# Performance work log

Hardware: AMD Instinct MI355X
Metric: run time of the kernel (lower is better)

The kernel has to match this reference:

```python
import math
import jax, jax.numpy as jnp
import numpy as np

BATCH, SEQ, D_MODEL, NUM_HEADS = 4, 2048, 1024, 16
D_K = D_MODEL // NUM_HEADS


def setup_inputs() -> dict:
    key = jax.random.key(0)
    ks = jax.random.split(key, 11)
    s = 0.02
    inp = {
        'encodings_q': jax.random.normal(ks[0], (BATCH, SEQ, D_MODEL), jnp.float32),
        'encodings_k': jax.random.normal(ks[1], (BATCH, SEQ, D_MODEL), jnp.float32),
        'encodings_v': jax.random.normal(ks[2], (BATCH, SEQ, D_MODEL), jnp.float32),
        # causal mask: True = masked out (matches masked_fill semantics)
        'mask': jnp.broadcast_to(jnp.triu(jnp.ones((SEQ, SEQ), bool), k=1),
                                 (BATCH, SEQ, SEQ)),
        'Wq': jax.random.normal(ks[3], (D_MODEL, D_MODEL), jnp.float32) * s,
        'bq': jnp.zeros((D_MODEL,), jnp.float32),
        'Wk': jax.random.normal(ks[4], (D_MODEL, D_MODEL), jnp.float32) * s,
        'bk': jnp.zeros((D_MODEL,), jnp.float32),
        'Wv': jax.random.normal(ks[5], (D_MODEL, D_MODEL), jnp.float32) * s,
        'bv': jnp.zeros((D_MODEL,), jnp.float32),
        'Wo': jax.random.normal(ks[6], (D_MODEL, D_MODEL), jnp.float32) * s,
        'bo': jnp.zeros((D_MODEL,), jnp.float32),
    }
    return inp


def reference(encodings_q, encodings_k, encodings_v, mask,
              Wq, bq, Wk, bk, Wv, bv, Wo, bo):
    B, S, D = encodings_q.shape
    H, Dk = NUM_HEADS, D_K
    # projections (nn.Linear: x @ W.T + b), split heads -> (B, H, S, Dk)
    q = (encodings_q @ Wq.T + bq).reshape(B, S, H, Dk).transpose(0, 2, 1, 3)
    k = (encodings_k @ Wk.T + bk).reshape(B, S, H, Dk).transpose(0, 2, 1, 3)
    v = (encodings_v @ Wv.T + bv).reshape(B, S, H, Dk).transpose(0, 2, 1, 3)
    scores = jnp.einsum('bhqd,bhkd->bhqk', q, k) / math.sqrt(Dk)
    # mask dim == 3 -> unsqueeze head dim; masked_fill(mask, -1e9)
    scores = jnp.where(mask[:, None, :, :], jnp.float32(-1e9), scores)
    weights = jax.nn.softmax(scores, axis=-1)
    attn = jnp.einsum('bhqk,bhkd->bhqd', weights, v)
    attn = attn.transpose(0, 2, 1, 3).reshape(B, S, D)
    return attn @ Wo.T + bo
```

## Files before the change

### kernel.cpp

```cpp
#include <hip/hip_runtime.h>
#include <hip/hip_bf16.h>
#include <cstdint>

typedef __bf16 bf16;
typedef bf16  bf16x4 __attribute__((ext_vector_type(4)));
typedef bf16  bf16x8 __attribute__((ext_vector_type(8)));
typedef float f32x4  __attribute__((ext_vector_type(4)));

#define MFMA16(a, b, c) __builtin_amdgcn_mfma_f32_16x16x32_bf16((a), (b), (c), 0, 0, 0)

constexpr int BATCH = 4;
constexpr int SEQ   = 2048;
constexpr int DM    = 1024;
constexpr int NH    = 16;
constexpr int DK    = 64;

__device__ __forceinline__ void gld_lds16(const void* g, void* l) {
    __builtin_amdgcn_global_load_lds(
        (const __attribute__((address_space(1))) unsigned int*)(uintptr_t)g,
        (__attribute__((address_space(3))) unsigned int*)(uintptr_t)l,
        16, 0, 0);
}

__device__ __forceinline__ bf16x8 cvt8(const float* __restrict__ p) {
    f32x4 a = *(const f32x4*)p;
    f32x4 b = *(const f32x4*)(p + 4);
    bf16x8 r;
    r[0] = (bf16)a[0]; r[1] = (bf16)a[1]; r[2] = (bf16)a[2]; r[3] = (bf16)a[3];
    r[4] = (bf16)b[0]; r[5] = (bf16)b[1]; r[6] = (bf16)b[2]; r[7] = (bf16)b[3];
    return r;
}

__global__ __launch_bounds__(256)
void cvt_all(const float* __restrict__ xq, const float* __restrict__ xk,
             const float* __restrict__ xv,
             const float* __restrict__ wq, const float* __restrict__ wk,
             const float* __restrict__ wv, const float* __restrict__ wo,
             bf16* __restrict__ X3, bf16* __restrict__ WB)
{
    const int bid = blockIdx.x;
    const float* s;
    bf16* d;
    int local;
    if (bid < 12288) {
        const int which = bid >> 12;
        local = bid & 4095;
        s = (which == 0) ? xq : (which == 1) ? xk : xv;
        d = X3 + (size_t)which * ((size_t)BATCH * SEQ * DM);
    } else {
        const int b2 = bid - 12288;
        const int which = b2 >> 9;
        local = b2 & 511;
        s = (which == 0) ? wq : (which == 1) ? wk : (which == 2) ? wv : wo;
        d = WB + (size_t)which * (size_t)(DM * DM);
    }
    const size_t i = ((size_t)local * 256 + threadIdx.x) * 8;
    *(bf16x8*)(d + i) = cvt8(s + i);
}

__global__ __launch_bounds__(256)
void cvt_x(const float* __restrict__ src, bf16* __restrict__ dst) {
    const size_t i = ((size_t)blockIdx.x * 256 + threadIdx.x) * 8;
    *(bf16x8*)(dst + i) = cvt8(src + i);
}

__global__ __launch_bounds__(256)
void cvt_w4(const float* __restrict__ s0, const float* __restrict__ s1,
            const float* __restrict__ s2, const float* __restrict__ s3,
            bf16* __restrict__ dst) {
    const float* s = (blockIdx.y == 0) ? s0 : (blockIdx.y == 1) ? s1
                   : (blockIdx.y == 2) ? s2 : s3;
    const size_t i = ((size_t)blockIdx.x * 256 + threadIdx.x) * 8;
    *(bf16x8*)(dst + (size_t)blockIdx.y * (1024 * 1024) + i) = cvt8(s + i);
}

template <int MODE>
__device__ __forceinline__
void gemm_core(const bf16* __restrict__ A, const bf16* __restrict__ W,
               const float* __restrict__ bias, void* __restrict__ outp,
               int m0, int n0, bf16* As, bf16* Bs)
{
    const int tid  = threadIdx.x;
    const int lane = tid & 63;
    const int wave = tid >> 6;
    const int wm   = (wave >> 1) * 64;
    const int wn   = (wave & 1) * 64;
    const int q4   = lane >> 4;
    const int r    = lane & 15;
    const int srow = lane >> 2;
    const int scol = (lane & 3) * 8;

    f32x4 acc[4][4];
#pragma unroll
    for (int i = 0; i < 4; i++)
#pragma unroll
        for (int j = 0; j < 4; j++) acc[i][j] = (f32x4){0.f, 0.f, 0.f, 0.f};

    const bf16* Ag = A + (size_t)(m0 + wave * 32 + srow) * 1024 + scol;
    const bf16* Wg = W + (size_t)(n0 + wave * 32 + srow) * 1024 + scol;
    bf16* AsB = &As[(wave * 32) * 32];
    bf16* BsB = &Bs[(wave * 32) * 32];

    for (int k0 = 0; k0 < 1024; k0 += 32) {
        __syncthreads();
        gld_lds16(Ag + k0,             AsB);
        gld_lds16(Ag + 16 * 1024 + k0, AsB + 16 * 32);
        gld_lds16(Wg + k0,             BsB);
        gld_lds16(Wg + 16 * 1024 + k0, BsB + 16 * 32);
        __syncthreads();

        bf16x8 af[4], bfr[4];
#pragma unroll
        for (int i = 0; i < 4; i++)
            af[i] = *(const bf16x8*)&As[(wm + i * 16 + r) * 32 + q4 * 8];
#pragma unroll
        for (int j = 0; j < 4; j++)
            bfr[j] = *(const bf16x8*)&Bs[(wn + j * 16 + r) * 32 + q4 * 8];
#pragma unroll
        for (int i = 0; i < 4; i++)
#pragma unroll
            for (int j = 0; j < 4; j++) {
                if (MODE == 2)
                    acc[i][j] = MFMA16(af[i], bfr[j], acc[i][j]);
                else
                    acc[i][j] = MFMA16(bfr[j], af[i], acc[i][j]);
            }
    }

    if (MODE == 2) {
#pragma unroll
        for (int j = 0; j < 4; j++) {
            const int col = n0 + wn + j * 16 + r;
            const float bv = bias[col];
            const int hh = col >> 6, d = col & 63;
#pragma unroll
            for (int i = 0; i < 4; i++) {
                const int s0 = m0 + wm + i * 16 + q4 * 4;
                const int b = s0 >> 11, s = s0 & 2047;
                bf16x4 ov;
#pragma unroll
                for (int rr = 0; rr < 4; rr++) ov[rr] = (bf16)(acc[i][j][rr] + bv);
                *(bf16x4*)&((bf16*)outp)[(((size_t)(b * NH + hh)) * DK + d) * SEQ + s] = ov;
            }
        }
    } else {
#pragma unroll
        for (int j = 0; j < 4; j++) {
            const int col0 = n0 + wn + j * 16 + q4 * 4;
            const f32x4 bv4 = *(const f32x4*)&bias[col0];
#pragma unroll
            for (int i = 0; i < 4; i++) {
                const int row = m0 + wm + i * 16 + r;
                if (MODE == 1) {
                    f32x4 ov = acc[i][j] + bv4;
                    *(f32x4*)&((float*)outp)[(size_t)row * 1024 + col0] = ov;
                } else {
                    const int b = row >> 11, s = row & 2047;
                    const int hh = col0 >> 6, d0 = col0 & 63;
                    bf16x4 ov;
#pragma unroll
                    for (int rr = 0; rr < 4; rr++) ov[rr] = (bf16)(acc[i][j][rr] + bv4[rr]);
                    *(bf16x4*)&((bf16*)outp)[(((size_t)(b * NH + hh)) * SEQ + s) * DK + d0] = ov;
                }
            }
        }
    }
}

template <int MODE>
__global__ __launch_bounds__(256)
void gemm_fast(const bf16* __restrict__ A, const bf16* __restrict__ W,
               const float* __restrict__ bias, void* __restrict__ outp)
{
    __shared__ __align__(16) bf16 As[128 * 32];
    __shared__ __align__(16) bf16 Bs[128 * 32];
    gemm_core<MODE>(A, W, bias, outp, blockIdx.x * 128, blockIdx.y * 128, As, Bs);
}

__global__ __launch_bounds__(256)
void gemm_qkv(const bf16* __restrict__ X3, const bf16* __restrict__ WB,
              const float* __restrict__ bq, const float* __restrict__ bk,
              const float* __restrict__ bv,
              bf16* __restrict__ Qt, bf16* __restrict__ Kt, bf16* __restrict__ Vt)
{
    __shared__ __align__(16) bf16 As[128 * 32];
    __shared__ __align__(16) bf16 Bs[128 * 32];
    const int z = blockIdx.z;
    const size_t E = (size_t)BATCH * SEQ * DM, WE = (size_t)DM * DM;
    const bf16* A = X3 + (size_t)z * E;
    const bf16* W = WB + (size_t)z * WE;
    const int m0 = blockIdx.x * 128, n0 = blockIdx.y * 128;
    if (z == 2)
        gemm_core<2>(A, W, bv, Vt, m0, n0, As, Bs);
    else if (z == 1)
        gemm_core<0>(A, W, bk, Kt, m0, n0, As, Bs);
    else
        gemm_core<0>(A, W, bq, Qt, m0, n0, As, Bs);
}

template <int MODE>
__global__ __launch_bounds__(256)
void gemm_slow(const void* __restrict__ Ap, const float* __restrict__ W,
               const float* __restrict__ bias, void* __restrict__ outp)
{
    __shared__ __align__(16) bf16 As[128 * 32];
    __shared__ __align__(16) bf16 Bs[128 * 32];

    const int tid  = threadIdx.x;
    const int lane = tid & 63;
    const int wave = tid >> 6;
    const int wm   = (wave >> 1) * 64;
    const int wn   = (wave & 1) * 64;
    const int m0   = blockIdx.y * 128;
    const int n0   = blockIdx.x * 128;
    const int q    = lane >> 4;
    const int r    = lane & 15;
    const int lrow  = tid >> 2;
    const int lcol8 = (tid & 3) * 8;

    f32x4 acc[4][4];
#pragma unroll
    for (int i = 0; i < 4; i++)
#pragma unroll
        for (int j = 0; j < 4; j++) acc[i][j] = (f32x4){0.f, 0.f, 0.f, 0.f};

    for (int k0 = 0; k0 < 1024; k0 += 32) {
        __syncthreads();
        if (MODE != 1) {
            const float* Af = (const float*)Ap;
            *(bf16x8*)&As[lrow * 32 + lcol8] =
                cvt8(&Af[(size_t)(m0 + lrow) * 1024 + k0 + lcol8]);
            *(bf16x8*)&As[(64 + lrow) * 32 + lcol8] =
                cvt8(&Af[(size_t)(m0 + 64 + lrow) * 1024 + k0 + lcol8]);
        } else {
            const bf16* Ab = (const bf16*)Ap;
            *(bf16x8*)&As[lrow * 32 + lcol8] =
                *(const bf16x8*)&Ab[(size_t)(m0 + lrow) * 1024 + k0 + lcol8];
            *(bf16x8*)&As[(64 + lrow) * 32 + lcol8] =
                *(const bf16x8*)&Ab[(size_t)(m0 + 64 + lrow) * 1024 + k0 + lcol8];
        }
        *(bf16x8*)&Bs[lrow * 32 + lcol8] =
            cvt8(&W[(size_t)(n0 + lrow) * 1024 + k0 + lcol8]);
        *(bf16x8*)&Bs[(64 + lrow) * 32 + lcol8] =
            cvt8(&W[(size_t)(n0 + 64 + lrow) * 1024 + k0 + lcol8]);
        __syncthreads();

        bf16x8 af[4], bfr[4];
#pragma unroll
        for (int i = 0; i < 4; i++)
            af[i] = *(const bf16x8*)&As[(wm + i * 16 + r) * 32 + q * 8];
#pragma unroll
        for (int j = 0; j < 4; j++)
            bfr[j] = *(const bf16x8*)&Bs[(wn + j * 16 + r) * 32 + q * 8];
#pragma unroll
        for (int i = 0; i < 4; i++)
#pragma unroll
            for (int j = 0; j < 4; j++)
                acc[i][j] = MFMA16(af[i], bfr[j], acc[i][j]);
    }

#pragma unroll
    for (int j = 0; j < 4; j++) {
        const int col = n0 + wn + j * 16 + r;
        const float bv = bias[col];
#pragma unroll
        for (int i = 0; i < 4; i++) {
#pragma unroll
            for (int rr = 0; rr < 4; rr++) {
                const int row = m0 + wm + i * 16 + q * 4 + rr;
                const float v = acc[i][j][rr] + bv;
                if (MODE == 1) {
                    ((float*)outp)[(size_t)row * 1024 + col] = v;
                } else {
                    const int b = row >> 11, s = row & 2047;
                    const int hh = col >> 6, d = col & 63;
                    if (MODE == 0)
                        ((bf16*)outp)[(((size_t)(b * NH + hh)) * SEQ + s) * DK + d] = (bf16)v;
                    else
                        ((bf16*)outp)[(((size_t)(b * NH + hh)) * DK + d) * SEQ + s] = (bf16)v;
                }
            }
        }
    }
}

__global__ __launch_bounds__(256)
void attn_causal(const bf16* __restrict__ Qt, const bf16* __restrict__ Kt,
                 const bf16* __restrict__ Vtt, bf16* __restrict__ Ob)
{
    constexpr int LDK = 72;
    __shared__ __align__(16) bf16 Ks[64 * LDK];
    __shared__ __align__(16) bf16 Vs[64 * LDK];
    __shared__ __align__(16) bf16 Ps[4][16 * LDK];

    const int tid  = threadIdx.x;
    const int lane = tid & 63;
    const int wave = tid >> 6;
    const int q4   = lane >> 4;
    const int r    = lane & 15;

    const int bh = blockIdx.x;
    const int qb = blockIdx.y * 64;
    const int b  = bh >> 4;
    const int h  = bh & 15;

    const bf16* Qp = Qt  + ((size_t)bh * SEQ + qb + wave * 16) * DK;
    const bf16* Kp = Kt  + (size_t)bh * SEQ * DK;
    const bf16* Vp = Vtt + (size_t)bh * DK * SEQ;

    bf16x8 qf0 = *(const bf16x8*)&Qp[r * DK + q4 * 8];
    bf16x8 qf1 = *(const bf16x8*)&Qp[r * DK + 32 + q4 * 8];
#pragma unroll
    for (int j = 0; j < 8; j++) {
        qf0[j] = (bf16)((float)qf0[j] * 0.125f);
        qf1[j] = (bf16)((float)qf1[j] * 0.125f);
    }

    bf16x8 ones;
#pragma unroll
    for (int j = 0; j < 8; j++) ones[j] = (bf16)1.0f;

    f32x4 o[4], o5;
#pragma unroll
    for (int i = 0; i < 4; i++) o[i] = (f32x4){0.f, 0.f, 0.f, 0.f};
    o5 = (f32x4){0.f, 0.f, 0.f, 0.f};
    float m_i = -1e30f;

    const int nT   = blockIdx.y + 1;
    const int lrow = tid >> 2;
    const int lcol = (tid & 3) * 16;
    const int qrow = qb + wave * 16 + r;

    for (int t = 0; t < nT; ++t) {
        const int kb = t * 64;
        __syncthreads();
        *(bf16x8*)&Ks[lrow * LDK + lcol] =
            *(const bf16x8*)&Kp[(size_t)(kb + lrow) * DK + lcol];
        *(bf16x8*)&Ks[lrow * LDK + lcol + 8] =
            *(const bf16x8*)&Kp[(size_t)(kb + lrow) * DK + lcol + 8];
        *(bf16x8*)&Vs[lrow * LDK + lcol] =
            *(const bf16x8*)&Vp[(size_t)lrow * SEQ + kb + lcol];
        *(bf16x8*)&Vs[lrow * LDK + lcol + 8] =
            *(const bf16x8*)&Vp[(size_t)lrow * SEQ + kb + lcol + 8];
        __syncthreads();

        f32x4 s[4];
#pragma unroll
        for (int n = 0; n < 4; n++) {
            bf16x8 k0 = *(const bf16x8*)&Ks[(n * 16 + r) * LDK + q4 * 8];
            bf16x8 k1 = *(const bf16x8*)&Ks[(n * 16 + r) * LDK + 32 + q4 * 8];
            f32x4 a = (f32x4){0.f, 0.f, 0.f, 0.f};
            a = MFMA16(k0, qf0, a);
            a = MFMA16(k1, qf1, a);
            s[n] = a;
        }

        float mx = -1e30f;
        if (t == nT - 1) {
#pragma unroll
            for (int n = 0; n < 4; n++) {
                const int c0 = kb + n * 16 + q4 * 4;
#pragma unroll
                for (int rr = 0; rr < 4; rr++) {
                    if (c0 + rr > qrow) s[n][rr] = -1e30f;
                    mx = fmaxf(mx, s[n][rr]);
                }
            }
        } else {
#pragma unroll
            for (int n = 0; n < 4; n++)
#pragma unroll
                for (int rr = 0; rr < 4; rr++)
                    mx = fmaxf(mx, s[n][rr]);
        }
        mx = fmaxf(mx, __shfl_xor(mx, 16, 64));
        mx = fmaxf(mx, __shfl_xor(mx, 32, 64));

        const float mn = fmaxf(m_i, mx);
        const float alpha = __expf(m_i - mn);
        m_i = mn;
#pragma unroll
        for (int n = 0; n < 4; n++)
#pragma unroll
            for (int rr = 0; rr < 4; rr++)
                o[n][rr] *= alpha;
#pragma unroll
        for (int rr = 0; rr < 4; rr++) o5[rr] *= alpha;

        bf16* Pw = &Ps[wave][0];
#pragma unroll
        for (int n = 0; n < 4; n++) {
            bf16x4 pv;
#pragma unroll
            for (int rr = 0; rr < 4; rr++)
                pv[rr] = (bf16)__expf(s[n][rr] - m_i);
            *(bf16x4*)&Pw[r * LDK + n * 16 + q4 * 4] = pv;
        }
        asm volatile("s_waitcnt lgkmcnt(0)" ::: "memory");

#pragma unroll
        for (int kk = 0; kk < 2; kk++) {
            bf16x8 pf = *(const bf16x8*)&Pw[r * LDK + kk * 32 + q4 * 8];
#pragma unroll
            for (int n = 0; n < 4; n++) {
                bf16x8 vf = *(const bf16x8*)&Vs[(n * 16 + r) * LDK + kk * 32 + q4 * 8];
                o[n] = MFMA16(vf, pf, o[n]);
            }
            o5 = MFMA16(ones, pf, o5);
        }
    }

    const float inv = 1.0f / o5[0];
#pragma unroll
    for (int n = 0; n < 4; n++) {
        bf16x4 ov;
#pragma unroll
        for (int rr = 0; rr < 4; rr++) ov[rr] = (bf16)(o[n][rr] * inv);
        *(bf16x4*)&Ob[((size_t)b * SEQ + qrow) * DM + h * DK + n * 16 + q4 * 4] = ov;
    }
}

extern "C" void kernel_launch(void* const* d_in, const int* in_sizes, int n_in,
                              void* d_out, int out_size, void* d_ws, size_t ws_size,
                              hipStream_t stream)
{
    const float* xq = (const float*)d_in[0];
    const float* xk = (const float*)d_in[1];
    const float* xv = (const float*)d_in[2];
    const float* Wq = (const float*)d_in[4];
    const float* bq = (const float*)d_in[5];
    const float* Wk = (const float*)d_in[6];
    const float* bk = (const float*)d_in[7];
    const float* Wv = (const float*)d_in[8];
    const float* bv = (const float*)d_in[9];
    const float* Wo = (const float*)d_in[10];
    const float* bo = (const float*)d_in[11];

    const size_t E  = (size_t)BATCH * SEQ * DM;
    const size_t WE = (size_t)DM * DM;
    bf16* Qt = (bf16*)d_ws;
    bf16* Kt = Qt + E;
    bf16* Vt = Kt + E;
    bf16* Ab = Vt + E;

    dim3 gblk(256);
    dim3 agrid(BATCH * NH, SEQ / 64);

    const size_t need_fused = (7 * E + 4 * WE) * sizeof(bf16);
    const size_t need_fast  = (5 * E + 4 * WE) * sizeof(bf16);

    if (ws_size >= need_fused) {
        bf16* X3 = Ab + E;
        bf16* WB = X3 + 3 * E;

        cvt_all<<<dim3(14336), gblk, 0, stream>>>(xq, xk, xv, Wq, Wk, Wv, Wo, X3, WB);

        gemm_qkv<<<dim3(64, 8, 3), gblk, 0, stream>>>(X3, WB, bq, bk, bv, Qt, Kt, Vt);

        attn_causal<<<agrid, gblk, 0, stream>>>(Qt, Kt, Vt, Ab);

        gemm_fast<1><<<dim3(64, 8), gblk, 0, stream>>>(Ab, WB + 3 * WE, bo, d_out);
    } else if (ws_size >= need_fast) {
        bf16* X  = Ab + E;
        bf16* WB = X + E;

        cvt_w4<<<dim3(512, 4), gblk, 0, stream>>>(Wq, Wk, Wv, Wo, WB);

        cvt_x<<<dim3(4096), gblk, 0, stream>>>(xq, X);
        gemm_fast<0><<<dim3(64, 8), gblk, 0, stream>>>(X, WB + 0 * WE, bq, Qt);
        cvt_x<<<dim3(4096), gblk, 0, stream>>>(xk, X);
        gemm_fast<0><<<dim3(64, 8), gblk, 0, stream>>>(X, WB + 1 * WE, bk, Kt);
        cvt_x<<<dim3(4096), gblk, 0, stream>>>(xv, X);
        gemm_fast<2><<<dim3(64, 8), gblk, 0, stream>>>(X, WB + 2 * WE, bv, Vt);

        attn_causal<<<agrid, gblk, 0, stream>>>(Qt, Kt, Vt, Ab);

        gemm_fast<1><<<dim3(64, 8), gblk, 0, stream>>>(Ab, WB + 3 * WE, bo, d_out);
    } else {
        dim3 ggrid_s(DM / 128, (BATCH * SEQ) / 128);
        gemm_slow<0><<<ggrid_s, gblk, 0, stream>>>(xq, Wq, bq, Qt);
        gemm_slow<0><<<ggrid_s, gblk, 0, stream>>>(xk, Wk, bk, Kt);
        gemm_slow<2><<<ggrid_s, gblk, 0, stream>>>(xv, Wv, bv, Vt);
        attn_causal<<<agrid, gblk, 0, stream>>>(Qt, Kt, Vt, Ab);
        gemm_slow<1><<<ggrid_s, gblk, 0, stream>>>(Ab, Wo, bo, d_out);
    }
}
```

Baseline: 373.6 us.

## Double-buffer K/V tiles with async LDS loads, fold softmax scale into Q

The attention kernel now prefetches the next K/V tile into a second LDS buffer using direct global-to-LDS loads. It stores the tiles in an XOR-swizzled layout instead of padded rows, which removes the second barrier per iteration. The softmax scale and log2(e) are folded into the Q projection epilogue so attention can use exp2 directly. Rescaling of the running max is skipped unless the max grows by more than 8, and s_setprio is raised around the MFMA sections. Costs are twice the K/V LDS footprint and slightly different rounding, since the scaled Q is stored in bf16.

```diff
diff --git a/kernel.cpp b/kernel.cpp
--- a/kernel.cpp
+++ b/kernel.cpp
@@ -14,6 +14,8 @@
 constexpr int DM    = 1024;
 constexpr int NH    = 16;
 constexpr int DK    = 64;
+
+constexpr float QSCALE = 0.125f * 1.44269504088896340736f;
 
 __device__ __forceinline__ void gld_lds16(const void* g, void* l) {
     __builtin_amdgcn_global_load_lds(
@@ -78,7 +80,7 @@
 __device__ __forceinline__
 void gemm_core(const bf16* __restrict__ A, const bf16* __restrict__ W,
                const float* __restrict__ bias, void* __restrict__ outp,
-               int m0, int n0, bf16* As, bf16* Bs)
+               int m0, int n0, bf16* As, bf16* Bs, float oscale)
 {
     const int tid  = threadIdx.x;
     const int lane = tid & 63;
@@ -139,7 +141,7 @@
                 const int b = s0 >> 11, s = s0 & 2047;
                 bf16x4 ov;
 #pragma unroll
-                for (int rr = 0; rr < 4; rr++) ov[rr] = (bf16)(acc[i][j][rr] + bv);
+                for (int rr = 0; rr < 4; rr++) ov[rr] = (bf16)((acc[i][j][rr] + bv) * oscale);
                 *(bf16x4*)&((bf16*)outp)[(((size_t)(b * NH + hh)) * DK + d) * SEQ + s] = ov;
             }
         }
@@ -152,14 +154,14 @@
             for (int i = 0; i < 4; i++) {
                 const int row = m0 + wm + i * 16 + r;
                 if (MODE == 1) {
-                    f32x4 ov = acc[i][j] + bv4;
+                    f32x4 ov = (acc[i][j] + bv4) * oscale;
                     *(f32x4*)&((float*)outp)[(size_t)row * 1024 + col0] = ov;
                 } else {
                     const int b = row >> 11, s = row & 2047;
                     const int hh = col0 >> 6, d0 = col0 & 63;
                     bf16x4 ov;
 #pragma unroll
-                    for (int rr = 0; rr < 4; rr++) ov[rr] = (bf16)(acc[i][j][rr] + bv4[rr]);
+                    for (int rr = 0; rr < 4; rr++) ov[rr] = (bf16)((acc[i][j][rr] + bv4[rr]) * oscale);
                     *(bf16x4*)&((bf16*)outp)[(((size_t)(b * NH + hh)) * SEQ + s) * DK + d0] = ov;
                 }
             }
@@ -170,11 +172,11 @@
 template <int MODE>
 __global__ __launch_bounds__(256)
 void gemm_fast(const bf16* __restrict__ A, const bf16* __restrict__ W,
-               const float* __restrict__ bias, void* __restrict__ outp)
+               const float* __restrict__ bias, void* __restrict__ outp, float oscale)
 {
     __shared__ __align__(16) bf16 As[128 * 32];
     __shared__ __align__(16) bf16 Bs[128 * 32];
-    gemm_core<MODE>(A, W, bias, outp, blockIdx.x * 128, blockIdx.y * 128, As, Bs);
+    gemm_core<MODE>(A, W, bias, outp, blockIdx.x * 128, blockIdx.y * 128, As, Bs, oscale);
 }
 
 __global__ __launch_bounds__(256)
@@ -191,17 +193,17 @@
     const bf16* W = WB + (size_t)z * WE;
     const int m0 = blockIdx.x * 128, n0 = blockIdx.y * 128;
     if (z == 2)
-        gemm_core<2>(A, W, bv, Vt, m0, n0, As, Bs);
+        gemm_core<2>(A, W, bv, Vt, m0, n0, As, Bs, 1.0f);
     else if (z == 1)
-        gemm_core<0>(A, W, bk, Kt, m0, n0, As, Bs);
+        gemm_core<0>(A, W, bk, Kt, m0, n0, As, Bs, 1.0f);
     else
-        gemm_core<0>(A, W, bq, Qt, m0, n0, As, Bs);
+        gemm_core<0>(A, W, bq, Qt, m0, n0, As, Bs, QSCALE);
 }
 
 template <int MODE>
 __global__ __launch_bounds__(256)
 void gemm_slow(const void* __restrict__ Ap, const float* __restrict__ W,
-               const float* __restrict__ bias, void* __restrict__ outp)
+               const float* __restrict__ bias, void* __restrict__ outp, float oscale)
 {
     __shared__ __align__(16) bf16 As[128 * 32];
     __shared__ __align__(16) bf16 Bs[128 * 32];
@@ -268,7 +270,7 @@
 #pragma unroll
             for (int rr = 0; rr < 4; rr++) {
                 const int row = m0 + wm + i * 16 + q * 4 + rr;
-                const float v = acc[i][j][rr] + bv;
+                const float v = (acc[i][j][rr] + bv) * oscale;
                 if (MODE == 1) {
                     ((float*)outp)[(size_t)row * 1024 + col] = v;
                 } else {
@@ -288,10 +290,10 @@
 void attn_causal(const bf16* __restrict__ Qt, const bf16* __restrict__ Kt,
                  const bf16* __restrict__ Vtt, bf16* __restrict__ Ob)
 {
-    constexpr int LDK = 72;
-    __shared__ __align__(16) bf16 Ks[64 * LDK];
-    __shared__ __align__(16) bf16 Vs[64 * LDK];
-    __shared__ __align__(16) bf16 Ps[4][16 * LDK];
+    constexpr int LDP = 72;
+    __shared__ __align__(16) bf16 Ks[2][64 * 64];
+    __shared__ __align__(16) bf16 Vs[2][64 * 64];
+    __shared__ __align__(16) bf16 Ps[4][16 * LDP];
 
     const int tid  = threadIdx.x;
     const int lane = tid & 63;
@@ -308,13 +310,8 @@
     const bf16* Kp = Kt  + (size_t)bh * SEQ * DK;
     const bf16* Vp = Vtt + (size_t)bh * DK * SEQ;
 
-    bf16x8 qf0 = *(const bf16x8*)&Qp[r * DK + q4 * 8];
-    bf16x8 qf1 = *(const bf16x8*)&Qp[r * DK + 32 + q4 * 8];
-#pragma unroll
-    for (int j = 0; j < 8; j++) {
-        qf0[j] = (bf16)((float)qf0[j] * 0.125f);
-        qf1[j] = (bf16)((float)qf1[j] * 0.125f);
-    }
+    const bf16x8 qf0 = *(const bf16x8*)&Qp[r * DK + q4 * 8];
+    const bf16x8 qf1 = *(const bf16x8*)&Qp[r * DK + 32 + q4 * 8];
 
     bf16x8 ones;
 #pragma unroll
@@ -327,34 +324,60 @@
     float m_i = -1e30f;
 
     const int nT   = blockIdx.y + 1;
-    const int lrow = tid >> 2;
-    const int lcol = (tid & 3) * 16;
     const int qrow = qb + wave * 16 + r;
 
+    const int srow = wave * 16 + (lane >> 3);
+    const int scol = ((lane & 7) ^ (srow & 7)) * 8;
+    const bf16* KgA = Kp + (size_t)srow * DK + scol;
+    const bf16* VgA = Vp + (size_t)srow * SEQ + scol;
+
+    const int sw    = r & 7;
+    const int koffA = r * 64 + ((q4)     ^ sw) * 8;
+    const int koffB = r * 64 + ((q4 + 4) ^ sw) * 8;
+
+    {
+        bf16* kd = &Ks[0][wave * 1024];
+        bf16* vd = &Vs[0][wave * 1024];
+        gld_lds16(KgA,           kd);
+        gld_lds16(KgA + 8 * DK,  kd + 512);
+        gld_lds16(VgA,           vd);
+        gld_lds16(VgA + 8 * SEQ, vd + 512);
+        KgA += 64 * DK;
+        VgA += 64;
+    }
+
+    int nbuf = 0;
     for (int t = 0; t < nT; ++t) {
-        const int kb = t * 64;
         __syncthreads();
-        *(bf16x8*)&Ks[lrow * LDK + lcol] =
-            *(const bf16x8*)&Kp[(size_t)(kb + lrow) * DK + lcol];
-        *(bf16x8*)&Ks[lrow * LDK + lcol + 8] =
-            *(const bf16x8*)&Kp[(size_t)(kb + lrow) * DK + lcol + 8];
-        *(bf16x8*)&Vs[lrow * LDK + lcol] =
-            *(const bf16x8*)&Vp[(size_t)lrow * SEQ + kb + lcol];
-        *(bf16x8*)&Vs[lrow * LDK + lcol + 8] =
-            *(const bf16x8*)&Vp[(size_t)lrow * SEQ + kb + lcol + 8];
-        __syncthreads();
+
+        const bf16* Kb = Ks[nbuf];
+        const bf16* Vb = Vs[nbuf];
+
+        if (t + 1 < nT) {
+            bf16* kd = &Ks[nbuf ^ 1][wave * 1024];
+            bf16* vd = &Vs[nbuf ^ 1][wave * 1024];
+            gld_lds16(KgA,           kd);
+            gld_lds16(KgA + 8 * DK,  kd + 512);
+            gld_lds16(VgA,           vd);
+            gld_lds16(VgA + 8 * SEQ, vd + 512);
+            KgA += 64 * DK;
+            VgA += 64;
+        }
 
         f32x4 s[4];
+        __builtin_amdgcn_s_setprio(1);
 #pragma unroll
         for (int n = 0; n < 4; n++) {
-            bf16x8 k0 = *(const bf16x8*)&Ks[(n * 16 + r) * LDK + q4 * 8];
-            bf16x8 k1 = *(const bf16x8*)&Ks[(n * 16 + r) * LDK + 32 + q4 * 8];
+            bf16x8 k0 = *(const bf16x8*)&Kb[koffA + n * 1024];
+            bf16x8 k1 = *(const bf16x8*)&Kb[koffB + n * 1024];
             f32x4 a = (f32x4){0.f, 0.f, 0.f, 0.f};
             a = MFMA16(k0, qf0, a);
             a = MFMA16(k1, qf1, a);
             s[n] = a;
         }
-
+        __builtin_amdgcn_s_setprio(0);
+
+        const int kb = t * 64;
         float mx = -1e30f;
         if (t == nT - 1) {
 #pragma unroll
@@ -376,16 +399,18 @@
         mx = fmaxf(mx, __shfl_xor(mx, 16, 64));
         mx = fmaxf(mx, __shfl_xor(mx, 32, 64));
 
-        const float mn = fmaxf(m_i, mx);
-        const float alpha = __expf(m_i - mn);
-        m_i = mn;
-#pragma unroll
-        for (int n = 0; n < 4; n++)
-#pragma unroll
-            for (int rr = 0; rr < 4; rr++)
-                o[n][rr] *= alpha;
-#pragma unroll
-        for (int rr = 0; rr < 4; rr++) o5[rr] *= alpha;
+        if (__any(mx > m_i + 8.0f)) {
+            const float mn    = fmaxf(m_i, mx);
+            const float alpha = __builtin_amdgcn_exp2f(m_i - mn);
+            m_i = mn;
+#pragma unroll
+            for (int n = 0; n < 4; n++)
+#pragma unroll
+                for (int rr = 0; rr < 4; rr++)
+                    o[n][rr] *= alpha;
+#pragma unroll
+            for (int rr = 0; rr < 4; rr++) o5[rr] *= alpha;
+        }
 
         bf16* Pw = &Ps[wave][0];
 #pragma unroll
@@ -393,21 +418,26 @@
             bf16x4 pv;
 #pragma unroll
             for (int rr = 0; rr < 4; rr++)
-                pv[rr] = (bf16)__expf(s[n][rr] - m_i);
-            *(bf16x4*)&Pw[r * LDK + n * 16 + q4 * 4] = pv;
+                pv[rr] = (bf16)__builtin_amdgcn_exp2f(s[n][rr] - m_i);
+            *(bf16x4*)&Pw[r * LDP + n * 16 + q4 * 4] = pv;
         }
         asm volatile("s_waitcnt lgkmcnt(0)" ::: "memory");
 
+        __builtin_amdgcn_s_setprio(1);
 #pragma unroll
         for (int kk = 0; kk < 2; kk++) {
-            bf16x8 pf = *(const bf16x8*)&Pw[r * LDK + kk * 32 + q4 * 8];
+            bf16x8 pf = *(const bf16x8*)&Pw[r * LDP + kk * 32 + q4 * 8];
+            const int vo = (kk == 0) ? koffA : koffB;
 #pragma unroll
             for (int n = 0; n < 4; n++) {
-                bf16x8 vf = *(const bf16x8*)&Vs[(n * 16 + r) * LDK + kk * 32 + q4 * 8];
+                bf16x8 vf = *(const bf16x8*)&Vb[vo + n * 1024];
                 o[n] = MFMA16(vf, pf, o[n]);
             }
             o5 = MFMA16(ones, pf, o5);
         }
+        __builtin_amdgcn_s_setprio(0);
+
+        nbuf ^= 1;
     }
 
     const float inv = 1.0f / o5[0];
@@ -459,7 +489,7 @@
 
         attn_causal<<<agrid, gblk, 0, stream>>>(Qt, Kt, Vt, Ab);
 
-        gemm_fast<1><<<dim3(64, 8), gblk, 0, stream>>>(Ab, WB + 3 * WE, bo, d_out);
+        gemm_fast<1><<<dim3(64, 8), gblk, 0, stream>>>(Ab, WB + 3 * WE, bo, d_out, 1.0f);
     } else if (ws_size >= need_fast) {
         bf16* X  = Ab + E;
         bf16* WB = X + E;
@@ -467,21 +497,21 @@
         cvt_w4<<<dim3(512, 4), gblk, 0, stream>>>(Wq, Wk, Wv, Wo, WB);
 
         cvt_x<<<dim3(4096), gblk, 0, stream>>>(xq, X);
-        gemm_fast<0><<<dim3(64, 8), gblk, 0, stream>>>(X, WB + 0 * WE, bq, Qt);
+        gemm_fast<0><<<dim3(64, 8), gblk, 0, stream>>>(X, WB + 0 * WE, bq, Qt, QSCALE);
         cvt_x<<<dim3(4096), gblk, 0, stream>>>(xk, X);
-        gemm_fast<0><<<dim3(64, 8), gblk, 0, stream>>>(X, WB + 1 * WE, bk, Kt);
+        gemm_fast<0><<<dim3(64, 8), gblk, 0, stream>>>(X, WB + 1 * WE, bk, Kt, 1.0f);
         cvt_x<<<dim3(4096), gblk, 0, stream>>>(xv, X);
-        gemm_fast<2><<<dim3(64, 8), gblk, 0, stream>>>(X, WB + 2 * WE, bv, Vt);
+        gemm_fast<2><<<dim3(64, 8), gblk, 0, stream>>>(X, WB + 2 * WE, bv, Vt, 1.0f);
 
         attn_causal<<<agrid, gblk, 0, stream>>>(Qt, Kt, Vt, Ab);
 
-        gemm_fast<1><<<dim3(64, 8), gblk, 0, stream>>>(Ab, WB + 3 * WE, bo, d_out);
+        gemm_fast<1><<<dim3(64, 8), gblk, 0, stream>>>(Ab, WB + 3 * WE, bo, d_out, 1.0f);
     } else {
         dim3 ggrid_s(DM / 128, (BATCH * SEQ) / 128);
-        gemm_slow<0><<<ggrid_s, gblk, 0, stream>>>(xq, Wq, bq, Qt);
-        gemm_slow<0><<<ggrid_s, gblk, 0, stream>>>(xk, Wk, bk, Kt);
-        gemm_slow<2><<<ggrid_s, gblk, 0, stream>>>(xv, Wv, bv, Vt);
+        gemm_slow<0><<<ggrid_s, gblk, 0, stream>>>(xq, Wq, bq, Qt, QSCALE);
+        gemm_slow<0><<<ggrid_s, gblk, 0, stream>>>(xk, Wk, bk, Kt, 1.0f);
+        gemm_slow<2><<<ggrid_s, gblk, 0, stream>>>(xv, Wv, bv, Vt, 1.0f);
         attn_causal<<<agrid, gblk, 0, stream>>>(Qt, Kt, Vt, Ab);
-        gemm_slow<1><<<ggrid_s, gblk, 0, stream>>>(Ab, Wo, bo, d_out);
-    }
-}
+        gemm_slow<1><<<ggrid_s, gblk, 0, stream>>>(Ab, Wo, bo, d_out, 1.0f);
+    }
+}
```

New measurement: 356.0 us. 1.05x faster.
